# Kernel optimization log

Measured on AMD Instinct MI355X. Metric: run time of the kernel, lower is better.

The kernel has to match this reference:

```python
import jax, jax.numpy as jnp
import numpy as np

THETA_ALPHA = 160.0  # spatial bandwidth of bilateral kernel
THETA_BETA = 3.0     # color bandwidth of bilateral kernel
THETA_GAMMA = 3.0    # spatial bandwidth of spatial kernel
NUM_ITERS = 5        # mean-field iterations


def setup_inputs() -> dict:
    key = jax.random.key(0)
    ks = jax.random.split(key, 5)
    B, H, W, C = 1, 80, 80, 21
    unaries = jax.random.normal(ks[0], (B, H, W, C), dtype=jnp.float32)
    image = jax.random.uniform(ks[1], (B, H, W, 3), dtype=jnp.float32) * 255.0
    spatial_w = jax.random.normal(ks[2], (C, C), dtype=jnp.float32) * 0.1 + jnp.eye(C)
    bilateral_w = jax.random.normal(ks[3], (C, C), dtype=jnp.float32) * 0.1 + jnp.eye(C)
    compat = jax.random.normal(ks[4], (C, C), dtype=jnp.float32) * 0.1 - jnp.eye(C)
    return {"unaries": unaries, "image": image, "spatial_w": spatial_w,
            "bilateral_w": bilateral_w, "compat": compat}


def _gauss_kernel(feat):
    # feat: [N, F] -> dense Gaussian affinity exp(-0.5*||f_i - f_j||^2), [N, N]
    sq = jnp.sum(feat * feat, axis=-1)
    d2 = sq[:, None] + sq[None, :] - 2.0 * (feat @ feat.T)
    return jnp.exp(-0.5 * jnp.maximum(d2, 0.0))


def reference(unaries, image, spatial_w, bilateral_w, compat):
    B, H, W, C = unaries.shape
    N = H * W
    yy, xx = jnp.meshgrid(jnp.arange(H, dtype=jnp.float32),
                          jnp.arange(W, dtype=jnp.float32), indexing="ij")
    pos = jnp.stack([yy, xx], axis=-1).reshape(N, 2)          # [N, 2]
    rgb = image.reshape(N, 3)
    feat_s = pos / THETA_GAMMA                                 # spatial kernel features
    feat_b = jnp.concatenate([pos / THETA_ALPHA, rgb / THETA_BETA], axis=-1)
    Ks = _gauss_kernel(feat_s)                                 # [N, N]
    Kb = _gauss_kernel(feat_b)                                 # [N, N]
    norm_s = jnp.sum(Ks, axis=-1, keepdims=True)               # splat-of-ones normalization
    norm_b = jnp.sum(Kb, axis=-1, keepdims=True)
    u = unaries.reshape(N, C)
    q = u
    for _ in range(NUM_ITERS):
        p = jax.nn.softmax(q, axis=-1)                         # [N, C]
        msg = (Ks @ p) / norm_s @ spatial_w.T + (Kb @ p) / norm_b @ bilateral_w.T
        q = u - msg @ compat.T                                 # compatibility transform
    return q.reshape(B, H, W, C)
```

## Files before the change

kernel.cpp:

```cpp
#include <hip/hip_runtime.h>


#define HH 80
#define WW 80
#define NPIX 6400
#define CC 21
#define PP 24
#define NITER 5
#define NCAP 32
#define SADGATE 23u
#define RAD 10

typedef short short8 __attribute__((ext_vector_type(8)));
union H8 { short8 v; unsigned short u[8]; };
union U4 { uint4 v; unsigned u[4]; };

__device__ __forceinline__ float bf2f(unsigned short h) {
    return __uint_as_float(((unsigned)h) << 16);
}
__device__ __forceinline__ unsigned short f2bf(float f) {
    unsigned u = __float_as_uint(f);
    return (unsigned short)((u + 0x7fffu + ((u >> 16) & 1u)) >> 16);
}

__global__ void __launch_bounds__(1024) nbr_kernel(const float* __restrict__ image,
        const float* __restrict__ unaries,
        const float* __restrict__ sw, const float* __restrict__ bw,
        const float* __restrict__ ct,
        unsigned* __restrict__ nbr_pk, int* __restrict__ nbr_cnt,
        float* __restrict__ inv_ns_g, float* __restrict__ csw_g, float* __restrict__ cbw_g,
        unsigned short* __restrict__ p0) {
    __shared__ unsigned int cimg[NPIX];
    __shared__ float Sl[HH];
    __shared__ int   njl[16][NCAP];
    __shared__ float nkl[16][NCAP];
    int tid = threadIdx.x;
    int bid = blockIdx.x;
    for (int px = tid; px < NPIX; px += 1024) {
        float r = image[px * 3 + 0], g = image[px * 3 + 1], b = image[px * 3 + 2];
        unsigned ur = (unsigned)(r + 0.5f), ug = (unsigned)(g + 0.5f), ub = (unsigned)(b + 0.5f);
        cimg[px] = ur | (ug << 8) | (ub << 16);
    }
    if (tid < HH) {
        float s = 0.f;
        float t = (float)tid;
        for (int tp = 0; tp < HH; ++tp) {
            float d = t - (float)tp;
            s += __expf(-d * d * (1.0f / 18.0f));
        }
        Sl[tid] = s;
    }
    if (bid == 0) {
        for (int idx = tid; idx < 2 * CC * CC; idx += 1024) {
            int m = idx % (CC * CC);
            int c = m / CC, k = m % CC;
            const float* wmat = (idx < CC * CC) ? sw : bw;
            float s = 0.f;
            for (int mm = 0; mm < CC; ++mm) s += ct[c * CC + mm] * wmat[mm * CC + k];
            if (idx < CC * CC) csw_g[m] = s; else cbw_g[m] = s;
        }
    }
    __syncthreads();
    int lane = tid & 63;
    int w = tid >> 6;
    int i = bid * 16 + w;
    unsigned ci = cimg[i];
    float eir = image[i * 3 + 0], eig = image[i * 3 + 1], eib = image[i * 3 + 2];
    float yi = (float)(i / WW), xi = (float)(i % WW);
    int base = 0;
    float ksum = 0.f;
    const uint4* cimg4 = (const uint4*)cimg;
    for (int j0 = 0; j0 < NPIX; j0 += 256) {
        U4 cj4; cj4.v = cimg4[(j0 >> 2) + lane];
        unsigned sd[4];
        #pragma unroll
        for (int q = 0; q < 4; ++q) {
#if __has_builtin(__builtin_amdgcn_sad_u8)
            sd[q] = __builtin_amdgcn_sad_u8(ci, cj4.u[q], 0u);
#else
            unsigned cj = cj4.u[q];
            int dr = (int)(ci & 255u) - (int)(cj & 255u);
            int dg = (int)((ci >> 8) & 255u) - (int)((cj >> 8) & 255u);
            int db = (int)((ci >> 16) & 255u) - (int)((cj >> 16) & 255u);
            sd[q] = (unsigned)(abs(dr) + abs(dg) + abs(db));
#endif
        }
        unsigned smin = min(min(sd[0], sd[1]), min(sd[2], sd[3]));
        if (__ballot(smin <= SADGATE) == 0ull) continue;
        #pragma unroll
        for (int q = 0; q < 4; ++q) {
            int j = j0 + lane * 4 + q;
            bool pass = (sd[q] <= SADGATE);
            unsigned long long mask = __ballot(pass);
            if (pass) {
                int slot = base + __popcll(mask & ((1ull << lane) - 1ull));
                if (slot < NCAP) {
                    float er = eir - image[j * 3 + 0];
                    float eg = eig - image[j * 3 + 1];
                    float eb = eib - image[j * 3 + 2];
                    float dy = (yi - (float)(j / WW)) * (1.0f / 160.0f);
                    float dx = (xi - (float)(j % WW)) * (1.0f / 160.0f);
                    float d2 = (er * er + eg * eg + eb * eb) * (1.0f / 9.0f) + dy * dy + dx * dx;
                    float kk = __expf(-0.5f * d2);
                    njl[w][slot] = j;
                    nkl[w][slot] = kk;
                    ksum += kk;
                }
            }
            base += (int)__popcll(mask);
        }
    }
    for (int off = 32; off > 0; off >>= 1) ksum += __shfl_down(ksum, off, 64);
    ksum = __shfl(ksum, 0, 64);
    int cnt = (base < NCAP) ? base : NCAP;
    float inv = 1.0f / ksum;
    if (lane < cnt) {
        unsigned kk16 = (unsigned)f2bf(nkl[w][lane] * inv);
        nbr_pk[i * NCAP + lane] = ((unsigned)njl[w][lane] << 16) | kk16;
    }
    if (lane == 0) {
        nbr_cnt[i] = cnt;
        inv_ns_g[i] = 1.0f / (Sl[(int)yi] * Sl[(int)xi]);
    }
    float v = (lane < CC) ? unaries[i * CC + lane] : -1e30f;
    float m = v;
    for (int off = 16; off > 0; off >>= 1) m = fmaxf(m, __shfl_down(m, off, 32));
    m = __shfl(m, 0, 32);
    float e = (lane < CC) ? __expf(v - m) : 0.f;
    float s = e;
    for (int off = 16; off > 0; off >>= 1) s += __shfl_down(s, off, 32);
    s = __shfl(s, 0, 32);
    if (lane < PP) p0[i * PP + lane] = (lane < CC) ? f2bf(e / s) : (unsigned short)0;
}

__global__ void __launch_bounds__(256) iter_kernel(const float* __restrict__ unaries,
        const unsigned short* __restrict__ pc,
        const unsigned* __restrict__ nbr_pk, const int* __restrict__ nbr_cnt,
        const float* __restrict__ inv_ns_g,
        const float* __restrict__ csw_g, const float* __restrict__ cbw_g,
        unsigned short* __restrict__ pn, float* __restrict__ out, int last) {
    __shared__ float gl[16];
    __shared__ float cy[2][28 * PP];

    int tid = threadIdx.x;
    int band = blockIdx.x & 7;
    int local = blockIdx.x >> 3;
    int y = band * 10 + local / 10;
    int x0 = (local % 10) * 8;
    int xs = (x0 - RAD > 0) ? x0 - RAD : 0;
    int xe = (x0 + 8 + RAD < WW) ? x0 + 8 + RAD : WW;
    int extw = xe - xs;
    const short8* pc8 = (const short8*)pc;

    int px = tid >> 5, c = tid & 31;
    int x = x0 + px;
    int i = y * WW + x;

    float wsw[CC], wbw[CC];
    if (c < CC) {
        #pragma unroll
        for (int k = 0; k < CC; ++k) { wsw[k] = csw_g[c * CC + k]; wbw[k] = cbw_g[c * CC + k]; }
    }
    int   cnt = nbr_cnt[i];
    unsigned pk = 0;
    if (c < cnt) pk = nbr_pk[i * NCAP + c];
    float inv_ns = inv_ns_g[i];
    float u_i = (c < CC) ? unaries[i * CC + c] : 0.f;

    if (tid < 16) { float d = (float)tid; gl[tid] = __expf(-d * d * (1.0f / 18.0f)); }
    if (tid < extw * 6) {
        int col = tid / 6, sub = tid % 6;
        int grp = sub >> 1, half = sub & 1;
        int xa = xs + col;
        int ys_ = (y - RAD > 0) ? y - RAD : 0;
        int ye_ = (y + RAD < HH - 1) ? y + RAD : HH - 1;
        float a[8] = {0, 0, 0, 0, 0, 0, 0, 0};
        for (int yp = ys_ + half; yp <= ye_; yp += 2) {
            float d = (float)(y - yp);
            float g = __expf(-d * d * (1.0f / 18.0f));
            H8 h; h.v = pc8[(yp * WW + xa) * 3 + grp];
            #pragma unroll
            for (int e = 0; e < 8; ++e) a[e] += g * bf2f(h.u[e]);
        }
        #pragma unroll
        for (int e = 0; e < 8; ++e) cy[half][col * PP + grp * 8 + e] = a[e];
    }
    __syncthreads();

    float as_v = 0.f;
    if (c < CC) {
        int q0 = (x - RAD > 0) ? x - RAD : 0;
        int q1 = (x + RAD < WW - 1) ? x + RAD : WW - 1;
        float s = 0.f;
        for (int xp = q0; xp <= q1; ++xp) {
            int d = x - xp; if (d < 0) d = -d;
            int a = (xp - xs) * PP + c;
            s += gl[d] * (cy[0][a] + cy[1][a]);
        }
        as_v = s * inv_ns;
    }
    float ab0 = 0.f, ab1 = 0.f;
    for (int n = 0; n + 1 < cnt; n += 2) {
        unsigned pa = __shfl(pk, n, 32);
        unsigned pb = __shfl(pk, n + 1, 32);
        int ja = (int)(pa >> 16), jb = (int)(pb >> 16);
        float ka = bf2f((unsigned short)(pa & 0xffffu));
        float kb = bf2f((unsigned short)(pb & 0xffffu));
        if (c < CC) {
            ab0 += ka * bf2f(pc[ja * PP + c]);
            ab1 += kb * bf2f(pc[jb * PP + c]);
        }
    }
    if (cnt & 1) {
        unsigned pa = __shfl(pk, cnt - 1, 32);
        int ja = (int)(pa >> 16);
        float ka = bf2f((unsigned short)(pa & 0xffffu));
        if (c < CC) ab0 += ka * bf2f(pc[ja * PP + c]);
    }
    float ab_v = ab0 + ab1;
    float m = 0.f;
    #pragma unroll
    for (int k = 0; k < CC; ++k) {
        float ak = __shfl(as_v, k, 32);
        float bk = __shfl(ab_v, k, 32);
        if (c < CC) m += wsw[k] * ak + wbw[k] * bk;
    }
    if (last) {
        if (c < CC) out[i * CC + c] = u_i - m;
    } else {
        float ev = (c < CC) ? __expf(u_i - m) : 0.f;
        float s = ev;
        #pragma unroll
        for (int off = 16; off > 0; off >>= 1) s += __shfl_xor(s, off, 32);
        if (c < PP) pn[i * PP + c] = f2bf(ev / s);
    }
}

extern "C" void kernel_launch(void* const* d_in, const int* in_sizes, int n_in,
                              void* d_out, int out_size, void* d_ws, size_t ws_size,
                              hipStream_t stream) {
    const float* unaries = (const float*)d_in[0];
    const float* image   = (const float*)d_in[1];
    const float* sw      = (const float*)d_in[2];
    const float* bw      = (const float*)d_in[3];
    const float* ct      = (const float*)d_in[4];
    float* out = (float*)d_out;

    char* ws = (char*)d_ws;
    size_t off = 0;
    auto alloc = [&](size_t bytes) -> char* {
        char* p = ws + off;
        off += (bytes + 255) & ~(size_t)255;
        return p;
    };
    unsigned* nbr_pk = (unsigned*)alloc((size_t)NPIX * NCAP * 4);
    int*   nbr_cnt   = (int*)alloc((size_t)NPIX * 4);
    float* inv_ns_g  = (float*)alloc((size_t)NPIX * 4);
    unsigned short* pA = (unsigned short*)alloc((size_t)NPIX * PP * 2 + 256);
    unsigned short* pB = (unsigned short*)alloc((size_t)NPIX * PP * 2 + 256);
    float* csw_g   = (float*)alloc(CC * CC * 4);
    float* cbw_g   = (float*)alloc(CC * CC * 4);
    (void)ws_size;

    nbr_kernel<<<400, 1024, 0, stream>>>(image, unaries, sw, bw, ct,
                                         nbr_pk, nbr_cnt, inv_ns_g,
                                         csw_g, cbw_g, pA);
    unsigned short* pc = pA;
    unsigned short* pn = pB;
    for (int t = 0; t < NITER; ++t) {
        iter_kernel<<<800, 256, 0, stream>>>(unaries, pc, nbr_pk, nbr_cnt,
                                             inv_ns_g, csw_g, cbw_g, pn, out,
                                             (t == NITER - 1) ? 1 : 0);
        unsigned short* tsw = pc; pc = pn; pn = tsw;
    }
}
```

Measured before the change: 131.1 us.

## Process two image rows per block to share vertical spatial-filter loads

```diff
diff --git a/kernel.cpp b/kernel.cpp
--- a/kernel.cpp
+++ b/kernel.cpp
@@ -133,26 +133,28 @@
     if (lane < PP) p0[i * PP + lane] = (lane < CC) ? f2bf(e / s) : (unsigned short)0;
 }
 
-__global__ void __launch_bounds__(256) iter_kernel(const float* __restrict__ unaries,
+__global__ void __launch_bounds__(512) iter_kernel(const float* __restrict__ unaries,
         const unsigned short* __restrict__ pc,
         const unsigned* __restrict__ nbr_pk, const int* __restrict__ nbr_cnt,
         const float* __restrict__ inv_ns_g,
         const float* __restrict__ csw_g, const float* __restrict__ cbw_g,
         unsigned short* __restrict__ pn, float* __restrict__ out, int last) {
     __shared__ float gl[16];
-    __shared__ float cy[2][28 * PP];
+    __shared__ float cy[2][2][28 * PP];
 
     int tid = threadIdx.x;
     int band = blockIdx.x & 7;
     int local = blockIdx.x >> 3;
-    int y = band * 10 + local / 10;
+    int y0 = band * 10 + (local / 10) * 2;
     int x0 = (local % 10) * 8;
     int xs = (x0 - RAD > 0) ? x0 - RAD : 0;
     int xe = (x0 + 8 + RAD < WW) ? x0 + 8 + RAD : WW;
     int extw = xe - xs;
     const short8* pc8 = (const short8*)pc;
 
-    int px = tid >> 5, c = tid & 31;
+    int grp_id = tid >> 5, c = tid & 31;
+    int row = grp_id >> 3, px = grp_id & 7;
+    int y = y0 + row;
     int x = x0 + px;
     int i = y * WW + x;
 
@@ -167,23 +169,34 @@
     float inv_ns = inv_ns_g[i];
     float u_i = (c < CC) ? unaries[i * CC + c] : 0.f;
 
-    if (tid < 16) { float d = (float)tid; gl[tid] = __expf(-d * d * (1.0f / 18.0f)); }
-    if (tid < extw * 6) {
-        int col = tid / 6, sub = tid % 6;
-        int grp = sub >> 1, half = sub & 1;
+    if (tid < 16) {
+        float d = (float)tid;
+        gl[tid] = (tid <= RAD) ? __expf(-d * d * (1.0f / 18.0f)) : 0.f;
+    }
+    if (tid >= 256 && tid < 256 + extw * 6) {
+        int t = tid - 256;
+        int col = t / 6, sub = t % 6;
+        int g8 = sub >> 1, half = sub & 1;
         int xa = xs + col;
-        int ys_ = (y - RAD > 0) ? y - RAD : 0;
-        int ye_ = (y + RAD < HH - 1) ? y + RAD : HH - 1;
-        float a[8] = {0, 0, 0, 0, 0, 0, 0, 0};
+        int ys_ = (y0 - RAD > 0) ? y0 - RAD : 0;
+        int ye_ = (y0 + 1 + RAD < HH - 1) ? y0 + 1 + RAD : HH - 1;
+        float a0[8] = {0, 0, 0, 0, 0, 0, 0, 0}, a1[8] = {0, 0, 0, 0, 0, 0, 0, 0};
         for (int yp = ys_ + half; yp <= ye_; yp += 2) {
-            float d = (float)(y - yp);
-            float g = __expf(-d * d * (1.0f / 18.0f));
-            H8 h; h.v = pc8[(yp * WW + xa) * 3 + grp];
+            int d0 = y0 - yp;     if (d0 < 0) d0 = -d0;
+            int d1 = y0 + 1 - yp; if (d1 < 0) d1 = -d1;
+            float g0 = gl[d0], g1 = gl[d1];
+            H8 h; h.v = pc8[(yp * WW + xa) * 3 + g8];
             #pragma unroll
-            for (int e = 0; e < 8; ++e) a[e] += g * bf2f(h.u[e]);
-        }
-        #pragma unroll
-        for (int e = 0; e < 8; ++e) cy[half][col * PP + grp * 8 + e] = a[e];
+            for (int e = 0; e < 8; ++e) {
+                float f = bf2f(h.u[e]);
+                a0[e] += g0 * f; a1[e] += g1 * f;
+            }
+        }
+        #pragma unroll
+        for (int e = 0; e < 8; ++e) {
+            cy[half][0][col * PP + g8 * 8 + e] = a0[e];
+            cy[half][1][col * PP + g8 * 8 + e] = a1[e];
+        }
     }
     __syncthreads();
 
@@ -195,7 +208,7 @@
         for (int xp = q0; xp <= q1; ++xp) {
             int d = x - xp; if (d < 0) d = -d;
             int a = (xp - xs) * PP + c;
-            s += gl[d] * (cy[0][a] + cy[1][a]);
+            s += gl[d] * (cy[0][row][a] + cy[1][row][a]);
         }
         as_v = s * inv_ns;
     }
@@ -268,7 +281,7 @@
     unsigned short* pc = pA;
     unsigned short* pn = pB;
     for (int t = 0; t < NITER; ++t) {
-        iter_kernel<<<800, 256, 0, stream>>>(unaries, pc, nbr_pk, nbr_cnt,
+        iter_kernel<<<400, 512, 0, stream>>>(unaries, pc, nbr_pk, nbr_cnt,
                                              inv_ns_g, csw_g, cbw_g, pn, out,
                                              (t == NITER - 1) ? 1 : 0);
         unsigned short* tsw = pc; pc = pn; pn = tsw;
```

Result: slower. 133.8 us (+2.0%).
